# Kernel tuning notes

Hardware: AMD Instinct MI355X
Metric: run time of the kernel (lower is better)

The kernel has to match this reference:

```python
import jax, jax.numpy as jnp
import numpy as np

STEP = 0.175
K = 128  # static bin cap; randn data at step 0.175 needs ~70 bins, so clipping is a no-op


def _bin_idx(x, step):
    # pd.cut(data, bins=arange(floor(min), ceil(max)+step, step)): interval (b[i], b[i+1]]
    # -> idx = ceil((x - lower)/step) - 1. Labels (bin midpoints) are bijective with idx,
    # so all downstream Counter/entropy math can run on integer bin indices directly.
    lower = jnp.floor(jnp.min(x))
    return jnp.clip(jnp.ceil((x - lower) / step) - 1, 0, K - 1).astype(jnp.int32)


def _row_entropy(codes):
    # plug-in Shannon entropy (natural log, like scipy.stats.entropy) per row:
    # H = log n - mean_j log(count of codes[j]); counts via sort + searchsorted runs
    s = jnp.sort(codes, axis=1)
    left = jax.vmap(lambda r: jnp.searchsorted(r, r, side='left'))(s)
    right = jax.vmap(lambda r: jnp.searchsorted(r, r, side='right'))(s)
    cnt = (right - left).astype(jnp.float32)
    return jnp.log(jnp.float32(codes.shape[1])) - jnp.mean(jnp.log(cnt), axis=1)


def _soft_ce(logits, target):
    # F.cross_entropy with soft targets, reduction='mean' (mean over batch)
    return jnp.mean(-jnp.sum(target * jax.nn.log_softmax(logits, -1), axis=-1))


def _kl_mean(logits, target):
    # F.kl_div(log_softmax(logits), target, reduction='mean') -> mean over ALL elements
    logp = jax.nn.log_softmax(logits, -1)
    return jnp.mean(target * (jnp.log(target) - logp))


def _H_out(logits, target):
    return _soft_ce(logits, target) - _kl_mean(logits, target)


def setup_inputs() -> dict:
    key = jax.random.key(0)
    ks = jax.random.split(key, 8)
    B, D = 4096, 1024
    return {
        'data': jax.random.normal(ks[0], (B, 3 * D), jnp.float32),
        'data1': jax.random.normal(ks[1], (B, D), jnp.float32),
        'data2': jax.random.normal(ks[2], (B, D), jnp.float32),
        'data3': jax.random.normal(ks[3], (B, D), jnp.float32),
        'output1': jax.random.normal(ks[4], (B, D), jnp.float32),
        'output2': jax.random.normal(ks[5], (B, D), jnp.float32),
        'output3': jax.random.normal(ks[6], (B, D), jnp.float32),
        'output': jax.random.normal(ks[7], (B, 3 * D), jnp.float32),
    }


def reference(data, data1, data2, data3, output1, output2, output3, output):
    cat = lambda xs: jnp.concatenate(xs, axis=1)
    mse = 0.5 * jnp.mean((data - output) ** 2)

    # discretized histogram/entropy path runs on .detach()'d numpy in torch -> stop_gradient
    i1 = _bin_idx(jax.lax.stop_gradient(data1), STEP)
    i2 = _bin_idx(jax.lax.stop_gradient(data2), STEP)
    i3 = _bin_idx(jax.lax.stop_gradient(data3), STEP)

    H_d1 = jnp.mean(_row_entropy(i1))
    H_d2 = jnp.mean(_row_entropy(i2))
    H_d3 = jnp.mean(_row_entropy(i3))

    p1 = jax.nn.softmax(data1, -1)
    p2 = jax.nn.softmax(data2, -1)
    p3 = jax.nn.softmax(data3, -1)
    H_o1 = _H_out(output1, p1)
    H_o2 = _H_out(output2, p2)
    H_o3 = _H_out(output3, p3)

    H_1 = H_d1 - H_o1
    H_2 = H_d2 - H_o2
    H_3 = H_d3 - H_o3

    # ave_joint_entropy over padded label matrices == joint entropy of (idx_x, idx_y) pairs
    # (equal column counts -> pad_matrices is a no-op; labels<->indices are bijective)
    H_in_13 = jnp.mean(_row_entropy(i1 * K + i3))
    H_in_23 = jnp.mean(_row_entropy(i2 * K + i3))
    H_in_12 = jnp.mean(_row_entropy(i1 * K + i2))

    H_o13 = _H_out(cat([output1, output3]), jax.nn.softmax(cat([data1, data3]), -1))
    H_o23 = _H_out(cat([output2, output3]), jax.nn.softmax(cat([data2, data3]), -1))
    H_o12 = _H_out(cat([output1, output2]), jax.nn.softmax(cat([data1, data2]), -1))

    H_MI13 = (H_o1 + H_o3 - H_o13) - (H_d1 + H_d3 - H_in_13)
    H_MI23 = (H_o2 + H_o3 - H_o23) - (H_d2 + H_d3 - H_in_23)
    H_MI12 = (H_o1 + H_o2 - H_o12) - (H_d1 + H_d2 - H_in_12)

    # per-row conditional MI I(x1; x2 | x3) = H(1,3)+H(2,3)-H(3)-H(1,2,3), SUMMED over rows
    c123 = (i1 * K + i2) * K + i3
    cmi_rows = (_row_entropy(i1 * K + i3) + _row_entropy(i2 * K + i3)
                - _row_entropy(i3) - _row_entropy(c123))
    data_mu = jnp.sum(cmi_rows)

    H_o123 = _H_out(cat([output1, output2, output3]),
                    jax.nn.softmax(cat([data1, data2, data3]), -1))
    label_cmi = H_o23 - H_o3 + H_o13 - H_o123
    CMI = label_cmi - data_mu

    return 0.9 * mse + 0.1 * (H_1 ** 2 + H_2 ** 2 + H_3 ** 2
                              + H_MI13 ** 2 + H_MI23 ** 2 + H_MI12 ** 2 + CMI ** 2)
```

## Files before the change

kernel.cpp:

```cpp
#include <hip/hip_runtime.h>
#include <stdint.h>

#define ROWS 4096
#define NCOL 1024
#define NT 256
#define NBANK 64
#define BSTRIDE 32

#define NB 72
#define ROWB 76
#define PAIRW (NB * (ROWB / 4))
#define TRIW 1536
#define T23_BASE PAIRW
#define T31_BASE (2 * PAIRW)
#define TRI_BASE (3 * PAIRW)
#define TABW (3 * PAIRW + TRIW)


__device__ __forceinline__ uint32_t f2ord(float f) {
  uint32_t b = __float_as_uint(f);
  return (b & 0x80000000u) ? ~b : (b | 0x80000000u);
}
__device__ __forceinline__ float ord2f(uint32_t u) {
  uint32_t b = (u & 0x80000000u) ? (u & 0x7FFFFFFFu) : ~u;
  return __uint_as_float(b);
}

__global__ __launch_bounds__(256) void k_pre(
    const float4* __restrict__ d1, const float4* __restrict__ d2,
    const float4* __restrict__ d3, uint32_t* __restrict__ minb) {
  __shared__ float sred[4];
  const int t = threadIdx.x;
  const float4* p = (blockIdx.y == 0) ? d1 : (blockIdx.y == 1) ? d2 : d3;
  const int n4 = ROWS * NCOL / 4;
  float lm = 1e30f;
  for (int i = blockIdx.x * 256 + t; i < n4; i += gridDim.x * 256) {
    float4 v = p[i];
    lm = fminf(lm, fminf(fminf(v.x, v.y), fminf(v.z, v.w)));
  }
  for (int o = 32; o > 0; o >>= 1) lm = fminf(lm, __shfl_down(lm, o, 64));
  if ((t & 63) == 0) sred[t >> 6] = lm;
  __syncthreads();
  if (t == 0) {
    lm = fminf(fminf(sred[0], sred[1]), fminf(sred[2], sred[3]));
    atomicMax(&minb[blockIdx.y], ~f2ord(lm));
  }
}

__device__ __noinline__ void hslow(uint32_t* __restrict__ tri, uint32_t key,
                                   uint32_t slot) {
  for (;;) {
    ++slot;
    if (slot == TRIW) slot = 0;
    uint32_t cur = tri[slot];
    if ((cur >> 11) == key) { atomicAdd((unsigned int*)&tri[slot], 1u); return; }
    if (cur == 0u) {
      uint32_t old = atomicCAS((unsigned int*)&tri[slot], 0u, (key << 11) | 1u);
      if (old == 0u) return;
      if ((old >> 11) == key) { atomicAdd((unsigned int*)&tri[slot], 1u); return; }
    }
  }
}

__device__ __forceinline__ uint32_t bini(float x, float low) {
  return (uint32_t)min(max((int)ceilf((x - low) * (1.0f / 0.175f)) - 1, 0),
                       NB - 1);
}

__global__ __launch_bounds__(NT, 7) void k_row(
    const float* __restrict__ d1, const float* __restrict__ d2,
    const float* __restrict__ d3, const float* __restrict__ o1,
    const float* __restrict__ o2, const float* __restrict__ o3,
    const float4* __restrict__ data, const float4* __restrict__ outp,
    const uint32_t* __restrict__ minb, float* __restrict__ acc) {
  __shared__ uint32_t tab[TABW];
  __shared__ float sA[4][12];
  __shared__ float sB[4][8];
  const int r = blockIdx.x, t = threadIdx.x;
  float* bank = acc + (r & (NBANK - 1)) * BSTRIDE;

#pragma unroll
  for (int i = t; i < TABW / 4; i += NT) ((uint4*)tab)[i] = make_uint4(0, 0, 0, 0);

  const float low1 = floorf(ord2f(~minb[0]));
  const float low2 = floorf(ord2f(~minb[1]));
  const float low3 = floorf(ord2f(~minb[2]));

  const size_t off = (size_t)r * NCOL;
  const float4 x1 = ((const float4*)(d1 + off))[t];
  const float4 x2 = ((const float4*)(d2 + off))[t];
  const float4 x3 = ((const float4*)(d3 + off))[t];
  const float xd[3][4] = {{x1.x, x1.y, x1.z, x1.w},
                          {x2.x, x2.y, x2.z, x2.w},
                          {x3.x, x3.y, x3.z, x3.w}};
  uint32_t b1[4], b2[4], b3[4];
#pragma unroll
  for (int u = 0; u < 4; ++u) {
    b1[u] = bini(xd[0][u], low1);
    b2[u] = bini(xd[1][u], low2);
    b3[u] = bini(xd[2][u], low3);
  }
  __syncthreads();

#pragma unroll
  for (int u = 0; u < 4; ++u) {
    const uint32_t i12 = b1[u] * ROWB + b2[u];
    const uint32_t i23 = b2[u] * ROWB + b3[u];
    const uint32_t i31 = b3[u] * ROWB + b1[u];
    atomicAdd((unsigned int*)&tab[i12 >> 2], 1u << ((i12 & 3u) * 8u));
    atomicAdd((unsigned int*)&tab[T23_BASE + (i23 >> 2)], 1u << ((i23 & 3u) * 8u));
    atomicAdd((unsigned int*)&tab[T31_BASE + (i31 >> 2)], 1u << ((i31 & 3u) * 8u));
  }

  const float4 y1 = ((const float4*)(o1 + off))[t];
  const float4 y2 = ((const float4*)(o2 + off))[t];
  const float4 y3 = ((const float4*)(o3 + off))[t];

  uint32_t key[4], slot[4], old[4];
#pragma unroll
  for (int u = 0; u < 4; ++u) {
    key[u] = (b1[u] << 14) | (b2[u] << 7) | b3[u];
    uint32_t h = (key[u] * 2654435761u) >> 21;
    slot[u] = (h * 3u) >> 2;
    old[u] = atomicCAS((unsigned int*)&tab[TRI_BASE + slot[u]], 0u,
                       (key[u] << 11) | 1u);
  }
#pragma unroll
  for (int u = 0; u < 4; ++u) {
    if (old[u] != 0u) {
      if ((old[u] >> 11) == key[u])
        atomicAdd((unsigned int*)&tab[TRI_BASE + slot[u]], 1u);
      else
        hslow(tab + TRI_BASE, key[u], slot[u]);
    }
  }

  float ms = 0.f;
  {
    const float4* pa = data + (size_t)r * 768;
    const float4* pb = outp + (size_t)r * 768;
#pragma unroll
    for (int u = 0; u < 3; ++u) {
      float4 a0 = pa[t + u * NT], bq = pb[t + u * NT];
      float dx = a0.x - bq.x, dy = a0.y - bq.y, dz = a0.z - bq.z, dw = a0.w - bq.w;
      ms += dx * dx + dy * dy + dz * dz + dw * dw;
    }
  }

  const float xo[3][4] = {{y1.x, y1.y, y1.z, y1.w},
                          {y2.x, y2.y, y2.z, y2.w},
                          {y3.x, y3.y, y3.z, y3.w}};
  float v[12];
#pragma unroll
  for (int k = 0; k < 3; ++k) {
    float E = 0.f, F = 0.f, G = 0.f, LE = 0.f;
#pragma unroll
    for (int u = 0; u < 4; ++u) {
      float w = __expf(xd[k][u]);
      E += w;
      F += w * xd[k][u];
      G += w * xo[k][u];
      LE += __expf(xo[k][u]);
    }
    v[k * 4 + 0] = E; v[k * 4 + 1] = F; v[k * 4 + 2] = G; v[k * 4 + 3] = LE;
  }
#pragma unroll
  for (int o = 32; o > 0; o >>= 1)
#pragma unroll
    for (int j = 0; j < 12; ++j) v[j] += __shfl_down(v[j], o, 64);
  if ((t & 63) == 0)
#pragma unroll
    for (int j = 0; j < 12; ++j) sA[t >> 6][j] = v[j];
  __syncthreads();

  float p[8] = {0.f, 0.f, 0.f, 0.f, 0.f, 0.f, 0.f, 0.f};
  p[7] = ms;
  if (t < 3 * NB) {
    const int tbl = t / NB, row = t - tbl * NB;
    const int pidx = (tbl == 0) ? 3 : (tbl == 1) ? 5 : 4;
    const uint32_t base = (uint32_t)tbl * PAIRW + (uint32_t)row * (ROWB / 4);
    uint32_t rowsum = 0;
    float pl = 0.f;
#pragma unroll
    for (int w = 0; w < 18; ++w) {
      uint32_t vv = tab[base + w];
      if (vv) {
        uint32_t s2 = (vv & 0x00FF00FFu) + ((vv >> 8) & 0x00FF00FFu);
        rowsum += (s2 + (s2 >> 16)) & 0xFFFFu;
#pragma unroll
        for (int bq = 0; bq < 4; ++bq) {
          uint32_t c = (vv >> (8 * bq)) & 255u;
          if (c > 1u) { float fc = (float)c; pl += fc * __logf(fc); }
        }
      }
    }
    p[pidx] = pl;
    if (rowsum > 1u) { float fr = (float)rowsum; p[tbl] = fr * __logf(fr); }
  }
  for (int i = t; i < TRIW / 4; i += NT) {
    uint4 e = ((const uint4*)(tab + TRI_BASE))[i];
    uint32_t c0 = e.x & 0x7FFu, c1 = e.y & 0x7FFu, c2 = e.z & 0x7FFu,
             c3 = e.w & 0x7FFu;
    if (c0 > 1u) { float fc = (float)c0; p[6] += fc * __logf(fc); }
    if (c1 > 1u) { float fc = (float)c1; p[6] += fc * __logf(fc); }
    if (c2 > 1u) { float fc = (float)c2; p[6] += fc * __logf(fc); }
    if (c3 > 1u) { float fc = (float)c3; p[6] += fc * __logf(fc); }
  }
#pragma unroll
  for (int o = 32; o > 0; o >>= 1)
#pragma unroll
    for (int j = 0; j < 8; ++j) p[j] += __shfl_down(p[j], o, 64);
  if ((t & 63) == 0)
#pragma unroll
    for (int j = 0; j < 8; ++j) sB[t >> 6][j] = p[j];
  __syncthreads();

  if (t < 16) {
    if (t < 7) {
      const int masks[7] = {1, 2, 4, 5, 6, 3, 7};
      const int m = masks[t];
      float Z = 0.f, Fs = 0.f, Gs = 0.f, LZ = 0.f;
#pragma unroll
      for (int k = 0; k < 3; ++k)
        if (m & (1 << k)) {
#pragma unroll
          for (int w = 0; w < 4; ++w) {
            Z += sA[w][k * 4 + 0];
            Fs += sA[w][k * 4 + 1];
            Gs += sA[w][k * 4 + 2];
            LZ += sA[w][k * 4 + 3];
          }
        }
      const float rZ = 1.0f / Z;
      const float T = Fs * rZ - __logf(Z);
      const float A = -(Gs * rZ) + __logf(LZ);
      atomicAdd(&bank[8 + t], A);
      atomicAdd(&bank[15 + t], T);
    } else if (t < 15) {
      const int j = t - 8;
      atomicAdd(&bank[1 + j], sB[0][j] + sB[1][j] + sB[2][j] + sB[3][j]);
    } else {
      atomicAdd(&bank[0], sB[0][7] + sB[1][7] + sB[2][7] + sB[3][7]);
    }
  }
}

__global__ void k_final(const float* __restrict__ acc, float* __restrict__ out) {
  const int t = threadIdx.x;
  double q[22];
#pragma unroll
  for (int i = 0; i < 22; ++i) q[i] = (double)acc[t * BSTRIDE + i];
#pragma unroll
  for (int o = 32; o > 0; o >>= 1)
#pragma unroll
    for (int i = 0; i < 22; ++i) q[i] += __shfl_down(q[i], o, 64);
  if (t != 0) return;

  const double logn = log(1024.0);
  const double Rn = 4096.0 * 1024.0;
  double Hd1 = logn - q[1] / Rn, Hd2 = logn - q[2] / Rn, Hd3 = logn - q[3] / Rn;
  double Hin12 = logn - q[4] / Rn, Hin13 = logn - q[5] / Rn, Hin23 = logn - q[6] / Rn;
  double data_mu = (q[3] + q[7] - q[5] - q[6]) / 1024.0;

  auto hout = [](double A, double T, double D) {
    return (1.0 - 1.0 / D) * A / 4096.0 - T / (4096.0 * D);
  };
  double Ho1 = hout(q[8], q[15], 1024.0);
  double Ho2 = hout(q[9], q[16], 1024.0);
  double Ho3 = hout(q[10], q[17], 1024.0);
  double Ho13 = hout(q[11], q[18], 2048.0);
  double Ho23 = hout(q[12], q[19], 2048.0);
  double Ho12 = hout(q[13], q[20], 2048.0);
  double Ho123 = hout(q[14], q[21], 3072.0);

  double H1 = Hd1 - Ho1, H2 = Hd2 - Ho2, H3 = Hd3 - Ho3;
  double MI13 = (Ho1 + Ho3 - Ho13) - (Hd1 + Hd3 - Hin13);
  double MI23 = (Ho2 + Ho3 - Ho23) - (Hd2 + Hd3 - Hin23);
  double MI12 = (Ho1 + Ho2 - Ho12) - (Hd1 + Hd2 - Hin12);
  double label_cmi = Ho23 - Ho3 + Ho13 - Ho123;
  double CMI = label_cmi - data_mu;
  double mse = 0.5 * q[0] / (4096.0 * 3072.0);
  out[0] = (float)(0.9 * mse +
                   0.1 * (H1 * H1 + H2 * H2 + H3 * H3 + MI13 * MI13 +
                          MI23 * MI23 + MI12 * MI12 + CMI * CMI));
}

extern "C" void kernel_launch(void* const* d_in, const int* in_sizes, int n_in,
                              void* d_out, int out_size, void* d_ws, size_t ws_size,
                              hipStream_t stream) {
  const float* data  = (const float*)d_in[0];
  const float* data1 = (const float*)d_in[1];
  const float* data2 = (const float*)d_in[2];
  const float* data3 = (const float*)d_in[3];
  const float* out1  = (const float*)d_in[4];
  const float* out2  = (const float*)d_in[5];
  const float* out3  = (const float*)d_in[6];
  const float* outp  = (const float*)d_in[7];
  float* acc = (float*)d_ws;
  uint32_t* minb = (uint32_t*)((float*)d_ws + NBANK * BSTRIDE);

  hipMemsetAsync(acc, 0, NBANK * BSTRIDE * sizeof(float) + 3 * sizeof(uint32_t),
                 stream);
  k_pre<<<dim3(256, 3), 256, 0, stream>>>((const float4*)data1,
                                          (const float4*)data2,
                                          (const float4*)data3, minb);
  k_row<<<ROWS, NT, 0, stream>>>(data1, data2, data3, out1, out2, out3,
                                 (const float4*)data, (const float4*)outp,
                                 minb, acc);
  k_final<<<1, 64, 0, stream>>>(acc, (float*)d_out);
}
```

Baseline: 241.6 us.

## Accumulate triple-table c·log c incrementally at insert; rebalance pair-row scan

Each atomic increment on the triple hash table now returns the previous count, and the thread adds the marginal change in c·log c right away. This removes the separate pass that scanned the whole triple table after the histogram was built. The pair-table scan now spreads rows from the centre outward across threads to even out the work. It also adds the packed byte words without masking and unpacks the row sum once at the end. The cost is up to two extra log calls per hashed element at insert time, which adds transcendental work to the hot path. Byte-wise summing of rs4 is only safe if no per-row byte total overflows 255.

```diff
diff --git a/kernel.cpp b/kernel.cpp
--- a/kernel.cpp
+++ b/kernel.cpp
@@ -47,17 +47,33 @@
   }
 }
 
-__device__ __noinline__ void hslow(uint32_t* __restrict__ tri, uint32_t key,
-                                   uint32_t slot) {
+__device__ __forceinline__ float marg_clogc(uint32_t prev) {
+  float f1 = (float)(prev + 1u);
+  float m = f1 * __logf(f1);
+  if (prev > 1u) {
+    float f0 = (float)prev;
+    m -= f0 * __logf(f0);
+  }
+  return m;
+}
+
+__device__ __noinline__ float hslow(uint32_t* __restrict__ tri, uint32_t key,
+                                    uint32_t slot) {
   for (;;) {
     ++slot;
     if (slot == TRIW) slot = 0;
     uint32_t cur = tri[slot];
-    if ((cur >> 11) == key) { atomicAdd((unsigned int*)&tri[slot], 1u); return; }
+    if (cur && (cur >> 11) == key) {
+      uint32_t prev = atomicAdd((unsigned int*)&tri[slot], 1u) & 0x7FFu;
+      return marg_clogc(prev);
+    }
     if (cur == 0u) {
       uint32_t old = atomicCAS((unsigned int*)&tri[slot], 0u, (key << 11) | 1u);
-      if (old == 0u) return;
-      if ((old >> 11) == key) { atomicAdd((unsigned int*)&tri[slot], 1u); return; }
+      if (old == 0u) return 0.f;
+      if ((old >> 11) == key) {
+        uint32_t prev = atomicAdd((unsigned int*)&tri[slot], 1u) & 0x7FFu;
+        return marg_clogc(prev);
+      }
     }
   }
 }
@@ -125,13 +141,17 @@
     old[u] = atomicCAS((unsigned int*)&tab[TRI_BASE + slot[u]], 0u,
                        (key[u] << 11) | 1u);
   }
+  float tripl = 0.f;
 #pragma unroll
   for (int u = 0; u < 4; ++u) {
     if (old[u] != 0u) {
-      if ((old[u] >> 11) == key[u])
-        atomicAdd((unsigned int*)&tab[TRI_BASE + slot[u]], 1u);
-      else
-        hslow(tab + TRI_BASE, key[u], slot[u]);
+      if ((old[u] >> 11) == key[u]) {
+        uint32_t prev =
+            atomicAdd((unsigned int*)&tab[TRI_BASE + slot[u]], 1u) & 0x7FFu;
+        tripl += marg_clogc(prev);
+      } else {
+        tripl += hslow(tab + TRI_BASE, key[u], slot[u]);
+      }
     }
   }
 
@@ -174,19 +194,22 @@
   __syncthreads();
 
   float p[8] = {0.f, 0.f, 0.f, 0.f, 0.f, 0.f, 0.f, 0.f};
+  p[6] = tripl;
   p[7] = ms;
   if (t < 3 * NB) {
-    const int tbl = t / NB, row = t - tbl * NB;
+    const int k = t / 3;
+    const int tbl = t - k * 3;
+    const int half = (k + 1) >> 1;
+    const int row = (k & 1) ? (35 + half) : (35 - half);
     const int pidx = (tbl == 0) ? 3 : (tbl == 1) ? 5 : 4;
     const uint32_t base = (uint32_t)tbl * PAIRW + (uint32_t)row * (ROWB / 4);
-    uint32_t rowsum = 0;
+    uint32_t rs4 = 0;
     float pl = 0.f;
 #pragma unroll
     for (int w = 0; w < 18; ++w) {
       uint32_t vv = tab[base + w];
-      if (vv) {
-        uint32_t s2 = (vv & 0x00FF00FFu) + ((vv >> 8) & 0x00FF00FFu);
-        rowsum += (s2 + (s2 >> 16)) & 0xFFFFu;
+      rs4 += vv;
+      if (vv & 0xFEFEFEFEu) {
 #pragma unroll
         for (int bq = 0; bq < 4; ++bq) {
           uint32_t c = (vv >> (8 * bq)) & 255u;
@@ -194,17 +217,10 @@
         }
       }
     }
+    uint32_t s2 = (rs4 & 0x00FF00FFu) + ((rs4 >> 8) & 0x00FF00FFu);
+    uint32_t rowsum = (s2 + (s2 >> 16)) & 0xFFFFu;
     p[pidx] = pl;
     if (rowsum > 1u) { float fr = (float)rowsum; p[tbl] = fr * __logf(fr); }
-  }
-  for (int i = t; i < TRIW / 4; i += NT) {
-    uint4 e = ((const uint4*)(tab + TRI_BASE))[i];
-    uint32_t c0 = e.x & 0x7FFu, c1 = e.y & 0x7FFu, c2 = e.z & 0x7FFu,
-             c3 = e.w & 0x7FFu;
-    if (c0 > 1u) { float fc = (float)c0; p[6] += fc * __logf(fc); }
-    if (c1 > 1u) { float fc = (float)c1; p[6] += fc * __logf(fc); }
-    if (c2 > 1u) { float fc = (float)c2; p[6] += fc * __logf(fc); }
-    if (c3 > 1u) { float fc = (float)c3; p[6] += fc * __logf(fc); }
   }
 #pragma unroll
   for (int o = 32; o > 0; o >>= 1)
```

Result: no change. 240.8 us (-0.3%).

## Hoist global loads, merge reductions into one DPP wave sum, simplify rowsum

Applied to the files above, without the earlier changes.

Issues all global loads (data/output rows for MSE, outputs for softmax) at kernel start before the LDS table zeroing, so memory latency overlaps the histogram work. The softmax sums and the entropy partials are merged into a single 20-value reduction done with DPP row and broadcast ops instead of shuffles, which removes one of the two shuffle reduction passes. Pair-table row sums now accumulate packed bytes and unpack once at the end, and the per-word log loop is skipped unless some byte is above 1. Holding more values in flight raises register pressure, which may reduce occupancy under launch bounds of 7 blocks.

```diff
diff --git a/kernel.cpp b/kernel.cpp
--- a/kernel.cpp
+++ b/kernel.cpp
@@ -24,6 +24,17 @@
 __device__ __forceinline__ float ord2f(uint32_t u) {
   uint32_t b = (u & 0x80000000u) ? (u & 0x7FFFFFFFu) : ~u;
   return __uint_as_float(b);
+}
+
+__device__ __forceinline__ float wave_sum(float x) {
+  float t;
+  t = __int_as_float(__builtin_amdgcn_update_dpp(0, __float_as_int(x), 0x111, 0xf, 0xf, false)); x += t;
+  t = __int_as_float(__builtin_amdgcn_update_dpp(0, __float_as_int(x), 0x112, 0xf, 0xf, false)); x += t;
+  t = __int_as_float(__builtin_amdgcn_update_dpp(0, __float_as_int(x), 0x114, 0xf, 0xf, false)); x += t;
+  t = __int_as_float(__builtin_amdgcn_update_dpp(0, __float_as_int(x), 0x118, 0xf, 0xf, false)); x += t;
+  t = __int_as_float(__builtin_amdgcn_update_dpp(0, __float_as_int(x), 0x142, 0xa, 0xf, false)); x += t;
+  t = __int_as_float(__builtin_amdgcn_update_dpp(0, __float_as_int(x), 0x143, 0xc, 0xf, false)); x += t;
+  return x;
 }
 
 __global__ __launch_bounds__(256) void k_pre(
@@ -73,23 +84,27 @@
     const float* __restrict__ o2, const float* __restrict__ o3,
     const float4* __restrict__ data, const float4* __restrict__ outp,
     const uint32_t* __restrict__ minb, float* __restrict__ acc) {
-  __shared__ uint32_t tab[TABW];
-  __shared__ float sA[4][12];
-  __shared__ float sB[4][8];
+  __shared__ __align__(16) uint32_t tab[TABW];
+  __shared__ float sAB[4][20];
   const int r = blockIdx.x, t = threadIdx.x;
   float* bank = acc + (r & (NBANK - 1)) * BSTRIDE;
-
-#pragma unroll
-  for (int i = t; i < TABW / 4; i += NT) ((uint4*)tab)[i] = make_uint4(0, 0, 0, 0);
-
-  const float low1 = floorf(ord2f(~minb[0]));
-  const float low2 = floorf(ord2f(~minb[1]));
-  const float low3 = floorf(ord2f(~minb[2]));
 
   const size_t off = (size_t)r * NCOL;
   const float4 x1 = ((const float4*)(d1 + off))[t];
   const float4 x2 = ((const float4*)(d2 + off))[t];
   const float4 x3 = ((const float4*)(d3 + off))[t];
+  const float4* pa = data + (size_t)r * 768;
+  const float4* pb = outp + (size_t)r * 768;
+  const float4 a0 = pa[t], a1 = pa[t + NT], a2 = pa[t + 2 * NT];
+  const float4 q0 = pb[t], q1 = pb[t + NT], q2 = pb[t + 2 * NT];
+
+#pragma unroll
+  for (int i = t; i < TABW / 4; i += NT) ((uint4*)tab)[i] = make_uint4(0, 0, 0, 0);
+
+  const float low1 = floorf(ord2f(~minb[0]));
+  const float low2 = floorf(ord2f(~minb[1]));
+  const float low3 = floorf(ord2f(~minb[2]));
+
   const float xd[3][4] = {{x1.x, x1.y, x1.z, x1.w},
                           {x2.x, x2.y, x2.z, x2.w},
                           {x3.x, x3.y, x3.z, x3.w}};
@@ -100,6 +115,38 @@
     b2[u] = bini(xd[1][u], low2);
     b3[u] = bini(xd[2][u], low3);
   }
+
+  float ms;
+  {
+    float dx = a0.x - q0.x, dy = a0.y - q0.y, dz = a0.z - q0.z, dw = a0.w - q0.w;
+    ms = dx * dx + dy * dy + dz * dz + dw * dw;
+    dx = a1.x - q1.x; dy = a1.y - q1.y; dz = a1.z - q1.z; dw = a1.w - q1.w;
+    ms += dx * dx + dy * dy + dz * dz + dw * dw;
+    dx = a2.x - q2.x; dy = a2.y - q2.y; dz = a2.z - q2.z; dw = a2.w - q2.w;
+    ms += dx * dx + dy * dy + dz * dz + dw * dw;
+  }
+
+  const float4 y1 = ((const float4*)(o1 + off))[t];
+  const float4 y2 = ((const float4*)(o2 + off))[t];
+  const float4 y3 = ((const float4*)(o3 + off))[t];
+  const float xo[3][4] = {{y1.x, y1.y, y1.z, y1.w},
+                          {y2.x, y2.y, y2.z, y2.w},
+                          {y3.x, y3.y, y3.z, y3.w}};
+  float v[12];
+#pragma unroll
+  for (int k = 0; k < 3; ++k) {
+    float E = 0.f, F = 0.f, G = 0.f, LE = 0.f;
+#pragma unroll
+    for (int u = 0; u < 4; ++u) {
+      float w = __expf(xd[k][u]);
+      E += w;
+      F += w * xd[k][u];
+      G += w * xo[k][u];
+      LE += __expf(xo[k][u]);
+    }
+    v[k * 4 + 0] = E; v[k * 4 + 1] = F; v[k * 4 + 2] = G; v[k * 4 + 3] = LE;
+  }
+
   __syncthreads();
 
 #pragma unroll
@@ -112,10 +159,6 @@
     atomicAdd((unsigned int*)&tab[T31_BASE + (i31 >> 2)], 1u << ((i31 & 3u) * 8u));
   }
 
-  const float4 y1 = ((const float4*)(o1 + off))[t];
-  const float4 y2 = ((const float4*)(o2 + off))[t];
-  const float4 y3 = ((const float4*)(o3 + off))[t];
-
   uint32_t key[4], slot[4], old[4];
 #pragma unroll
   for (int u = 0; u < 4; ++u) {
@@ -135,58 +178,25 @@
     }
   }
 
-  float ms = 0.f;
-  {
-    const float4* pa = data + (size_t)r * 768;
-    const float4* pb = outp + (size_t)r * 768;
-#pragma unroll
-    for (int u = 0; u < 3; ++u) {
-      float4 a0 = pa[t + u * NT], bq = pb[t + u * NT];
-      float dx = a0.x - bq.x, dy = a0.y - bq.y, dz = a0.z - bq.z, dw = a0.w - bq.w;
-      ms += dx * dx + dy * dy + dz * dz + dw * dw;
-    }
-  }
-
-  const float xo[3][4] = {{y1.x, y1.y, y1.z, y1.w},
-                          {y2.x, y2.y, y2.z, y2.w},
-                          {y3.x, y3.y, y3.z, y3.w}};
-  float v[12];
-#pragma unroll
-  for (int k = 0; k < 3; ++k) {
-    float E = 0.f, F = 0.f, G = 0.f, LE = 0.f;
-#pragma unroll
-    for (int u = 0; u < 4; ++u) {
-      float w = __expf(xd[k][u]);
-      E += w;
-      F += w * xd[k][u];
-      G += w * xo[k][u];
-      LE += __expf(xo[k][u]);
-    }
-    v[k * 4 + 0] = E; v[k * 4 + 1] = F; v[k * 4 + 2] = G; v[k * 4 + 3] = LE;
-  }
-#pragma unroll
-  for (int o = 32; o > 0; o >>= 1)
-#pragma unroll
-    for (int j = 0; j < 12; ++j) v[j] += __shfl_down(v[j], o, 64);
-  if ((t & 63) == 0)
-#pragma unroll
-    for (int j = 0; j < 12; ++j) sA[t >> 6][j] = v[j];
   __syncthreads();
 
-  float p[8] = {0.f, 0.f, 0.f, 0.f, 0.f, 0.f, 0.f, 0.f};
-  p[7] = ms;
+  float p[20];
+#pragma unroll
+  for (int j = 0; j < 12; ++j) p[j] = v[j];
+#pragma unroll
+  for (int j = 12; j < 19; ++j) p[j] = 0.f;
+  p[19] = ms;
   if (t < 3 * NB) {
     const int tbl = t / NB, row = t - tbl * NB;
     const int pidx = (tbl == 0) ? 3 : (tbl == 1) ? 5 : 4;
     const uint32_t base = (uint32_t)tbl * PAIRW + (uint32_t)row * (ROWB / 4);
-    uint32_t rowsum = 0;
+    uint32_t rs4 = 0;
     float pl = 0.f;
 #pragma unroll
     for (int w = 0; w < 18; ++w) {
       uint32_t vv = tab[base + w];
-      if (vv) {
-        uint32_t s2 = (vv & 0x00FF00FFu) + ((vv >> 8) & 0x00FF00FFu);
-        rowsum += (s2 + (s2 >> 16)) & 0xFFFFu;
+      rs4 += vv;
+      if (vv & 0xFEFEFEFEu) {
 #pragma unroll
         for (int bq = 0; bq < 4; ++bq) {
           uint32_t c = (vv >> (8 * bq)) & 255u;
@@ -194,25 +204,26 @@
         }
       }
     }
-    p[pidx] = pl;
-    if (rowsum > 1u) { float fr = (float)rowsum; p[tbl] = fr * __logf(fr); }
+    uint32_t s2 = (rs4 & 0x00FF00FFu) + ((rs4 >> 8) & 0x00FF00FFu);
+    uint32_t rowsum = (s2 + (s2 >> 16)) & 0xFFFFu;
+    p[12 + pidx] = pl;
+    if (rowsum > 1u) { float fr = (float)rowsum; p[12 + tbl] = fr * __logf(fr); }
   }
   for (int i = t; i < TRIW / 4; i += NT) {
     uint4 e = ((const uint4*)(tab + TRI_BASE))[i];
     uint32_t c0 = e.x & 0x7FFu, c1 = e.y & 0x7FFu, c2 = e.z & 0x7FFu,
              c3 = e.w & 0x7FFu;
-    if (c0 > 1u) { float fc = (float)c0; p[6] += fc * __logf(fc); }
-    if (c1 > 1u) { float fc = (float)c1; p[6] += fc * __logf(fc); }
-    if (c2 > 1u) { float fc = (float)c2; p[6] += fc * __logf(fc); }
-    if (c3 > 1u) { float fc = (float)c3; p[6] += fc * __logf(fc); }
-  }
-#pragma unroll
-  for (int o = 32; o > 0; o >>= 1)
-#pragma unroll
-    for (int j = 0; j < 8; ++j) p[j] += __shfl_down(p[j], o, 64);
-  if ((t & 63) == 0)
-#pragma unroll
-    for (int j = 0; j < 8; ++j) sB[t >> 6][j] = p[j];
+    if (c0 > 1u) { float fc = (float)c0; p[18] += fc * __logf(fc); }
+    if (c1 > 1u) { float fc = (float)c1; p[18] += fc * __logf(fc); }
+    if (c2 > 1u) { float fc = (float)c2; p[18] += fc * __logf(fc); }
+    if (c3 > 1u) { float fc = (float)c3; p[18] += fc * __logf(fc); }
+  }
+
+#pragma unroll
+  for (int j = 0; j < 20; ++j) p[j] = wave_sum(p[j]);
+  if ((t & 63) == 63)
+#pragma unroll
+    for (int j = 0; j < 20; ++j) sAB[t >> 6][j] = p[j];
   __syncthreads();
 
   if (t < 16) {
@@ -225,10 +236,10 @@
         if (m & (1 << k)) {
 #pragma unroll
           for (int w = 0; w < 4; ++w) {
-            Z += sA[w][k * 4 + 0];
-            Fs += sA[w][k * 4 + 1];
-            Gs += sA[w][k * 4 + 2];
-            LZ += sA[w][k * 4 + 3];
+            Z += sAB[w][k * 4 + 0];
+            Fs += sAB[w][k * 4 + 1];
+            Gs += sAB[w][k * 4 + 2];
+            LZ += sAB[w][k * 4 + 3];
           }
         }
       const float rZ = 1.0f / Z;
@@ -238,9 +249,10 @@
       atomicAdd(&bank[15 + t], T);
     } else if (t < 15) {
       const int j = t - 8;
-      atomicAdd(&bank[1 + j], sB[0][j] + sB[1][j] + sB[2][j] + sB[3][j]);
+      atomicAdd(&bank[1 + j],
+                sAB[0][12 + j] + sAB[1][12 + j] + sAB[2][12 + j] + sAB[3][12 + j]);
     } else {
-      atomicAdd(&bank[0], sB[0][7] + sB[1][7] + sB[2][7] + sB[3][7]);
+      atomicAdd(&bank[0], sAB[0][19] + sAB[1][19] + sAB[2][19] + sAB[3][19]);
     }
   }
 }
```

New measurement: 299.2 us. +23.8%, slower.
